# Performance work log

Hardware: AMD Instinct MI355X
Metric: run time of the kernel (lower is better)

Reference implementation:

```python
import jax, jax.numpy as jnp
import numpy as np

T, B, U, A, H, K, G = 800, 128, 64, 64, 256, 10, 20
IN1, IN2, IN3 = 3 + A, 3 + A + H, 3 + A + H


def _lstm_cell(x, h, c, W_ih, W_hh, b):
    # PyTorch LSTMCell: gates in order i, f, g, o
    z = x @ W_ih.T + h @ W_hh.T + b
    i, f, g, o = jnp.split(z, 4, axis=-1)
    c_new = jax.nn.sigmoid(f) * c + jax.nn.sigmoid(i) * jnp.tanh(g)
    h_new = jax.nn.sigmoid(o) * jnp.tanh(c_new)
    return h_new, c_new


def setup_inputs() -> dict:
    key = jax.random.key(0)
    ks = jax.random.split(key, 32)
    s = 0.08
    p = {}
    p['x'] = jax.random.normal(ks[0], (T, B, 3), jnp.float32)
    p['c'] = jax.random.uniform(ks[1], (B, U, A), jnp.float32)
    p['W1_ih'] = jax.random.normal(ks[2], (4 * H, IN1), jnp.float32) * s
    p['W1_hh'] = jax.random.normal(ks[3], (4 * H, H), jnp.float32) * s
    p['b1'] = jax.random.normal(ks[4], (4 * H,), jnp.float32) * s
    p['W2_ih'] = jax.random.normal(ks[5], (4 * H, IN2), jnp.float32) * s
    p['W2_hh'] = jax.random.normal(ks[6], (4 * H, H), jnp.float32) * s
    p['b2'] = jax.random.normal(ks[7], (4 * H,), jnp.float32) * s
    p['W3_ih'] = jax.random.normal(ks[8], (4 * H, IN3), jnp.float32) * s
    p['W3_hh'] = jax.random.normal(ks[9], (4 * H, H), jnp.float32) * s
    p['b3'] = jax.random.normal(ks[10], (4 * H,), jnp.float32) * s
    p['Ww'] = jax.random.normal(ks[11], (3 * K, H), jnp.float32) * s
    p['bw'] = jax.random.normal(ks[12], (3 * K,), jnp.float32) * s
    p['We'] = jax.random.normal(ks[13], (1, H), jnp.float32) * s
    p['be'] = jax.random.normal(ks[14], (1,), jnp.float32) * s
    p['Wpi'] = jax.random.normal(ks[15], (G, H), jnp.float32) * s
    p['bpi'] = jax.random.normal(ks[16], (G,), jnp.float32) * s
    p['Wm1'] = jax.random.normal(ks[17], (G, H), jnp.float32) * s
    p['bm1'] = jax.random.normal(ks[18], (G,), jnp.float32) * s
    p['Wm2'] = jax.random.normal(ks[19], (G, H), jnp.float32) * s
    p['bm2'] = jax.random.normal(ks[20], (G,), jnp.float32) * s
    p['Ws1'] = jax.random.normal(ks[21], (G, H), jnp.float32) * s
    p['bs1'] = jax.random.normal(ks[22], (G,), jnp.float32) * s
    p['Ws2'] = jax.random.normal(ks[23], (G, H), jnp.float32) * s
    p['bs2'] = jax.random.normal(ks[24], (G,), jnp.float32) * s
    p['Wr'] = jax.random.normal(ks[25], (G, H), jnp.float32) * s
    p['br'] = jax.random.normal(ks[26], (G,), jnp.float32) * s
    return p


def reference(x, c, W1_ih, W1_hh, b1, W2_ih, W2_hh, b2, W3_ih, W3_hh, b3,
              Ww, bw, We, be, Wpi, bpi, Wm1, bm1, Wm2, bm2,
              Ws1, bs1, Ws2, bs2, Wr, br):
    u = jnp.arange(U, dtype=x.dtype)  # character positions

    def step(carry, x_t):
        h1, c1, h2, c2, h3, c3, w, kappa = carry
        h1, c1 = _lstm_cell(jnp.concatenate([x_t, w], 1), h1, c1, W1_ih, W1_hh, b1)
        win = jnp.exp(h1 @ Ww.T + bw)                     # [B, 3K]
        alpha, beta, k = jnp.split(win, 3, axis=1)
        kappa = 0.1 * k + kappa                           # [B, K]
        # Phi[b,u] = sum_k alpha * exp(-beta * (kappa - u)^2)
        d = kappa[:, None, :] - u[None, :, None]          # [B, U, K]
        phi = jnp.sum(alpha[:, None, :] * jnp.exp(-beta[:, None, :] * d * d), -1)  # [B, U]
        w = jnp.einsum('bu,bua->ba', phi, c)              # [B, A]
        h2, c2 = _lstm_cell(jnp.concatenate([x_t, w, h1], 1), h2, c2, W2_ih, W2_hh, b2)
        h3, c3 = _lstm_cell(jnp.concatenate([x_t, w, h2], 1), h3, c3, W3_ih, W3_hh, b3)
        return (h1, c1, h2, c2, h3, c3, w, kappa), h3

    z = jnp.zeros((B, H), x.dtype)
    init = (z, z, z, z, z, z, jnp.ones((B, A), x.dtype), jnp.zeros((B, K), x.dtype))
    _, out = jax.lax.scan(step, init, x)                  # out: [T, B, H]

    es = jax.nn.sigmoid(-(out @ We.T + be)).squeeze(-1)   # 1/(1+exp(z)) == sigmoid(-z)
    pis = jax.nn.softmax(out @ Wpi.T + bpi, axis=2)
    mu1s = out @ Wm1.T + bm1
    mu2s = out @ Wm2.T + bm2
    sigma1s = jnp.exp(out @ Ws1.T + bs1)
    sigma2s = jnp.exp(out @ Ws2.T + bs2)
    rhos = jnp.tanh(out @ Wr.T + br)
    return es, pis, mu1s, mu2s, sigma1s, sigma2s, rhos
```

## Files before the change

kernel.cpp:

```cpp
#include <hip/hip_runtime.h>
#include <utility>

#define TT 800
#define BB 128
#define HH 256
#define UU 64
#define AA 64
#define KK 10
#define GG 20
#define NWG 256
#define GB 32
#define NGRP 4

typedef float f32x4 __attribute__((ext_vector_type(4)));
typedef __bf16 bf16y8 __attribute__((ext_vector_type(8)));
typedef short bf16s8 __attribute__((ext_vector_type(8)));
typedef unsigned long long u64x2 __attribute__((ext_vector_type(2)));

__device__ __forceinline__ float bf2f(unsigned short u) {
  return __uint_as_float(((unsigned int)u) << 16);
}
__device__ __forceinline__ unsigned short f2bf(float f) {
  unsigned int x = __float_as_uint(f);
  x += 0x7FFFu + ((x >> 16) & 1u);
  return (unsigned short)(x >> 16);
}
__device__ __forceinline__ unsigned packf(float v) {
  unsigned short hi = f2bf(v);
  unsigned short lo = f2bf(v - bf2f(hi));
  return (unsigned)hi | ((unsigned)lo << 16);
}
__device__ __forceinline__ float unpackf(unsigned u) {
  return bf2f((unsigned short)(u & 0xFFFF)) + bf2f((unsigned short)(u >> 16));
}
__device__ __forceinline__ float sigm(float x) { return 1.0f / (1.0f + __expf(-x)); }
__device__ __forceinline__ float rin(const void* p, size_t i, bool f32) {
  return f32 ? ((const float*)p)[i] : bf2f(((const unsigned short*)p)[i]);
}
__device__ __forceinline__ bf16y8 ld8(const unsigned short* p) {
  return __builtin_bit_cast(bf16y8, *(const bf16s8*)p);
}

__device__ __forceinline__ unsigned ald(const unsigned* p) {
  return __hip_atomic_load(p, __ATOMIC_RELAXED, __HIP_MEMORY_SCOPE_AGENT);
}
__device__ __forceinline__ void ast(unsigned* p, unsigned v) {
  __hip_atomic_store(p, v, __ATOMIC_RELAXED, __HIP_MEMORY_SCOPE_AGENT);
}

__device__ __forceinline__ void ld16(u64x2& d, const unsigned* p) {
  asm volatile("global_load_dwordx4 %0, %1, off sc0 sc1" : "=v"(d) : "v"(p));
}
template <int N>
__device__ __forceinline__ void waitvm() {
  asm volatile("s_waitcnt vmcnt(%0)" :: "i"(N) : "memory");
  __builtin_amdgcn_sched_barrier(0);
}

template <typename F, int... I>
__device__ __forceinline__ void unroll_seq(F&& f, std::integer_sequence<int, I...>) {
  (f(std::integral_constant<int, I>{}), ...);
}


struct KArgs {
  const void* in[27];
  float* out;
  float* kappa;
  unsigned *xu;
  unsigned *wu;
  unsigned *h1[2], *h2[2], *h3[2];
  unsigned* bar;
};

__device__ void fillB(unsigned short* Bhi, unsigned short* Blo, const void* Wih,
                      const void* Whh, int KP, int ihCols, int ihEnd, int hhStart,
                      int q, int tid, bool f32) {
  int total = KP * 16;
  for (int idx = tid; idx < total; idx += 256) {
    int k = idx >> 4, n = idx & 15;
    int row = (n >> 2) * HH + q * 4 + (n & 3);
    float v = 0.f;
    if (k < 3) v = rin(Wih, (size_t)row * ihCols + k, f32);
    else if (k >= 8 && k < ihEnd) v = rin(Wih, (size_t)row * ihCols + (k - 5), f32);
    else if (k >= hhStart && k < hhStart + 256) v = rin(Whh, (size_t)row * HH + (k - hhStart), f32);
    unsigned short hi = f2bf(v);
    int a = ((k >> 3) * 16 + n) * 8 + (k & 7);
    Bhi[a] = hi;
    Blo[a] = f2bf(v - bf2f(hi));
  }
}

template <int KC, bool R3, int WB>
__device__ __forceinline__ void gate_mfma(
    const unsigned* __restrict__ xt, const unsigned* __restrict__ wu,
    const unsigned* __restrict__ r2, const unsigned* __restrict__ r3,
    const unsigned* __restrict__ dz,
    const unsigned short* __restrict__ Bhi, const unsigned short* __restrict__ Blo,
    const float* __restrict__ bias4, float& creg, unsigned* __restrict__ hout,
    int grp, int q, float* zls, int tid) {
  const int wave = tid >> 6, lane = tid & 63;
  if ((wave >> 1) != (WB >> 1)) return;
  const int wv = wave & 1;
  const int n15 = lane & 15, quad = lane >> 4;
  const int b = grp * GB + wv * 16 + n15;

  unsigned xv0 = 0, xv1 = 0, xv2 = 0;
  if (quad == 0) {
    xv0 = xt[b * 3 + 0];
    xv1 = xt[b * 3 + 1];
    xv2 = xt[b * 3 + 2];
  }
  asm volatile("" :: "v"(xv0), "v"(xv1), "v"(xv2));

  constexpr int DEP = 12;
  u64x2 buf[DEP][2];

  auto addr = [&](int kc) -> const unsigned* {
    const int k0 = kc * 32 + quad * 8;
    if (kc == 0 && quad == 0) return dz;
    if (k0 < 72) return wu + ((k0 - 8) >> 3) * 1024 + b * 8;
    if (k0 < 328) return r2 + ((k0 - 72) >> 3) * 1024 + b * 8;
    if (R3 && k0 < 584) return r3 + ((k0 - 328) >> 3) * 1024 + b * 8;
    return dz;
  };
  auto issue = [&](int kc, int slot) {
    const unsigned* p = addr(kc);
    ld16(buf[slot][0], p);
    ld16(buf[slot][1], p + 4);
  };

#pragma unroll
  for (int kc = 0; kc < DEP && kc < KC; ++kc) issue(kc, kc);

  f32x4 acc = {0.f, 0.f, 0.f, 0.f};

  unroll_seq([&](auto kcc) {
    constexpr int kc = decltype(kcc)::value;
    constexpr int end = (kc + DEP < KC) ? (kc + DEP) : KC;
    waitvm<2 * (end - kc - 1)>();
    u64x2* sp = buf[kc % DEP];
    unsigned long long s[4] = { sp[0][0], sp[0][1], sp[1][0], sp[1][1] };
    bf16s8 th, tl;
#pragma unroll
    for (int j = 0; j < 4; ++j) {
      unsigned lo32 = (unsigned)s[j], hi32 = (unsigned)(s[j] >> 32);
      th[2 * j] = (short)(lo32 & 0xFFFFu);     tl[2 * j] = (short)(lo32 >> 16);
      th[2 * j + 1] = (short)(hi32 & 0xFFFFu); tl[2 * j + 1] = (short)(hi32 >> 16);
    }
    if constexpr (kc == 0) {
      if (quad == 0) {
        th[0] = (short)(xv0 & 0xFFFFu); tl[0] = (short)(xv0 >> 16);
        th[1] = (short)(xv1 & 0xFFFFu); tl[1] = (short)(xv1 >> 16);
        th[2] = (short)(xv2 & 0xFFFFu); tl[2] = (short)(xv2 >> 16);
      }
    }
    bf16y8 ah = __builtin_bit_cast(bf16y8, th);
    bf16y8 al = __builtin_bit_cast(bf16y8, tl);
    const int boff = ((kc * 4 + quad) * 16 + n15) * 8;
    bf16y8 bh = ld8(Bhi + boff), bl = ld8(Blo + boff);
    acc = __builtin_amdgcn_mfma_f32_16x16x32_bf16(ah, bh, acc, 0, 0, 0);
    acc = __builtin_amdgcn_mfma_f32_16x16x32_bf16(ah, bl, acc, 0, 0, 0);
    acc = __builtin_amdgcn_mfma_f32_16x16x32_bf16(al, bh, acc, 0, 0, 0);
    if constexpr (kc + DEP < KC) issue(kc + DEP, kc % DEP);
  }, std::make_integer_sequence<int, KC>{});

  float* zw = zls + wave * (16 * 17);
#pragma unroll
  for (int r = 0; r < 4; ++r) zw[(quad * 4 + r) * 17 + n15] = acc[r];
  const int m = lane >> 2, j = lane & 3;
  const int hu = q * 4 + j;
  const int bb = grp * GB + wv * 16 + m;
  float zi = zw[m * 17 + (0 + j)]  + bias4[0];
  float zf = zw[m * 17 + (4 + j)]  + bias4[1];
  float zg = zw[m * 17 + (8 + j)]  + bias4[2];
  float zo = zw[m * 17 + (12 + j)] + bias4[3];
  float cn = sigm(zf) * creg + sigm(zi) * tanhf(zg);
  creg = cn;
  float hn = sigm(zo) * tanhf(cn);
  ast(hout + (hu >> 3) * 1024 + bb * 8 + (hu & 7), packf(hn));
}

template <int kc> constexpr int lw_wait() {
  return kc == 0 ? 4 : kc == 1 ? 2 : kc == 2 ? 0 :
         kc == 15 ? 6 : kc == 16 ? 4 : kc == 17 ? 2 : kc == 18 ? 0 : -1;
}
__device__ __forceinline__ void gate_mfma_lw(
    const unsigned* __restrict__ xt, const unsigned* __restrict__ wu,
    const unsigned* __restrict__ r2, const unsigned* __restrict__ r3,
    const unsigned* __restrict__ dz,
    const unsigned short* __restrict__ Bhi, const unsigned short* __restrict__ Blo,
    const float* __restrict__ bias4, float& creg, unsigned* __restrict__ hout,
    const unsigned* __restrict__ afl, unsigned tgt,
    int grp, int q, float* zls, int tid) {
  constexpr int KC = 19, DEP = 12;
  const int wave = tid >> 6, lane = tid & 63;
  if (wave >= 2) return;
  const int wv = wave & 1;
  const int n15 = lane & 15, quad = lane >> 4;
  const int b = grp * GB + wv * 16 + n15;

  unsigned xv0 = 0, xv1 = 0, xv2 = 0;
  if (quad == 0) {
    xv0 = xt[b * 3 + 0];
    xv1 = xt[b * 3 + 1];
    xv2 = xt[b * 3 + 2];
  }
  asm volatile("" :: "v"(xv0), "v"(xv1), "v"(xv2));

  u64x2 buf[DEP][2];
  u64x2 wbuf[3][2];

  auto addr = [&](int kc) -> const unsigned* {
    const int k0 = kc * 32 + quad * 8;
    if (kc == 0 && quad == 0) return dz;
    if (k0 < 72) return wu + ((k0 - 8) >> 3) * 1024 + b * 8;
    if (k0 < 328) return r2 + ((k0 - 72) >> 3) * 1024 + b * 8;
    if (k0 < 584) return r3 + ((k0 - 328) >> 3) * 1024 + b * 8;
    return dz;
  };
  auto issue = [&](int kc, int slot) {
    const unsigned* p = addr(kc);
    ld16(buf[slot][0], p);
    ld16(buf[slot][1], p + 4);
  };

#pragma unroll
  for (int kc = 3; kc < 15; ++kc) issue(kc, kc % DEP);

  {
    const unsigned* fp = afl + (lane & 31) * 32;
    unsigned v = ald(fp);
    while (v < tgt) { __builtin_amdgcn_s_sleep(1); v = ald(fp); }
  }

#pragma unroll
  for (int kc = 0; kc < 3; ++kc) {
    const unsigned* p = addr(kc);
    ld16(wbuf[kc][0], p);
    ld16(wbuf[kc][1], p + 4);
  }

  f32x4 acc = {0.f, 0.f, 0.f, 0.f};

  unroll_seq([&](auto kcc) {
    constexpr int kc = decltype(kcc)::value;
    constexpr int wn = lw_wait<kc>();
    if constexpr (wn >= 0) waitvm<wn>();
    u64x2* sp = (kc < 3) ? wbuf[kc] : buf[kc % DEP];
    unsigned long long s[4] = { sp[0][0], sp[0][1], sp[1][0], sp[1][1] };
    bf16s8 th, tl;
#pragma unroll
    for (int j = 0; j < 4; ++j) {
      unsigned lo32 = (unsigned)s[j], hi32 = (unsigned)(s[j] >> 32);
      th[2 * j] = (short)(lo32 & 0xFFFFu);     tl[2 * j] = (short)(lo32 >> 16);
      th[2 * j + 1] = (short)(hi32 & 0xFFFFu); tl[2 * j + 1] = (short)(hi32 >> 16);
    }
    if constexpr (kc == 0) {
      if (quad == 0) {
        th[0] = (short)(xv0 & 0xFFFFu); tl[0] = (short)(xv0 >> 16);
        th[1] = (short)(xv1 & 0xFFFFu); tl[1] = (short)(xv1 >> 16);
        th[2] = (short)(xv2 & 0xFFFFu); tl[2] = (short)(xv2 >> 16);
      }
    }
    bf16y8 ah = __builtin_bit_cast(bf16y8, th);
    bf16y8 al = __builtin_bit_cast(bf16y8, tl);
    const int boff = ((kc * 4 + quad) * 16 + n15) * 8;
    bf16y8 bh = ld8(Bhi + boff), bl = ld8(Blo + boff);
    acc = __builtin_amdgcn_mfma_f32_16x16x32_bf16(ah, bh, acc, 0, 0, 0);
    acc = __builtin_amdgcn_mfma_f32_16x16x32_bf16(ah, bl, acc, 0, 0, 0);
    acc = __builtin_amdgcn_mfma_f32_16x16x32_bf16(al, bh, acc, 0, 0, 0);
    if constexpr (kc >= 3 && kc + DEP < KC) issue(kc + DEP, kc % DEP);
  }, std::make_integer_sequence<int, KC>{});

  float* zw = zls + wave * (16 * 17);
#pragma unroll
  for (int r = 0; r < 4; ++r) zw[(quad * 4 + r) * 17 + n15] = acc[r];
  const int m = lane >> 2, j = lane & 3;
  const int hu = q * 4 + j;
  const int bb = grp * GB + wv * 16 + m;
  float zi = zw[m * 17 + (0 + j)]  + bias4[0];
  float zf = zw[m * 17 + (4 + j)]  + bias4[1];
  float zg = zw[m * 17 + (8 + j)]  + bias4[2];
  float zo = zw[m * 17 + (12 + j)] + bias4[3];
  float cn = sigm(zf) * creg + sigm(zi) * tanhf(zg);
  creg = cn;
  float hn = sigm(zo) * tanhf(cn);
  ast(hout + (hu >> 3) * 1024 + bb * 8 + (hu & 7), packf(hn));
}

template <bool F32>
__device__ void window_stage(const KArgs& a, int b, const unsigned* __restrict__ h1c,
                             int tid, float* misc) {
  float* slab = misc;
  float* part = misc + 264;
  float* win  = misc + 508;
  float* kap  = misc + 538;
  float* phi  = misc + 552;
  const int wave = tid >> 6, lane = tid & 63;
  if (wave == 0) {
    const unsigned* p = h1c + (lane >> 1) * 1024 + b * 8 + (lane & 1) * 4;
    u64x2 d;
    ld16(d, p);
    waitvm<0>();
    const int hu0 = (lane >> 1) * 8 + (lane & 1) * 4;
    float* s4 = slab + (hu0 >> 5) * 33 + (hu0 & 31);
    s4[0] = unpackf((unsigned)d[0]);
    s4[1] = unpackf((unsigned)(d[0] >> 32));
    s4[2] = unpackf((unsigned)d[1]);
    s4[3] = unpackf((unsigned)(d[1] >> 32));
  }
  __syncthreads();
  if (tid < 240) {
    int r = tid >> 3, pp = tid & 7;
    const float* hh = slab + pp * 33;
    float s = 0.f;
    if (F32) {
      const f32x4* w4 = (const f32x4*)((const float*)a.in[11] + (size_t)r * HH + pp * 32);
#pragma unroll
      for (int j = 0; j < 8; ++j) {
        f32x4 v = w4[j];
        s += v[0] * hh[4 * j];     s += v[1] * hh[4 * j + 1];
        s += v[2] * hh[4 * j + 2]; s += v[3] * hh[4 * j + 3];
      }
    } else {
      const unsigned short* wr = (const unsigned short*)a.in[11] + (size_t)r * HH + pp * 32;
#pragma unroll
      for (int j = 0; j < 4; ++j) {
        bf16s8 v = *(const bf16s8*)(wr + 8 * j);
#pragma unroll
        for (int e = 0; e < 8; ++e) s += bf2f((unsigned short)v[e]) * hh[8 * j + e];
      }
    }
    part[tid] = s;
  }
  __syncthreads();
  if (tid < 30) {
    float s = rin(a.in[12], tid, F32);
#pragma unroll
    for (int i = 0; i < 8; ++i) s += part[tid * 8 + i];
    win[tid] = __expf(s);
  }
  __syncthreads();
  if (tid < 10) {
    float kp = a.kappa[b * KK + tid] + 0.1f * win[20 + tid];
    a.kappa[b * KK + tid] = kp;
    kap[tid] = kp;
  }
  __syncthreads();
  if (tid < 64) {
    float u = (float)tid, s = 0.f;
#pragma unroll
    for (int r = 0; r < 10; ++r) {
      float d = kap[r] - u;
      s += win[r] * __expf(-win[10 + r] * d * d);
    }
    phi[tid] = s;
  }
  __syncthreads();
  if (tid < 64) {
    float s = 0.f;
    for (int u = 0; u < 64; ++u) s += phi[u] * rin(a.in[1], ((size_t)b * UU + u) * AA + tid, F32);
    ast(a.wu + (tid >> 3) * 1024 + b * 8 + (tid & 7), packf(s));
  }
}

template <bool F32>
__device__ void proj_stage(const KArgs& a, int tt, const unsigned* __restrict__ h3b,
                           int b, int tid, float* misc) {
  float* shm  = misc;
  float* part = misc + 256;
  float* zp   = misc + 500;
  const int wave = tid >> 6, lane = tid & 63;
  if (wave == 0) {
    const unsigned* p = h3b + (lane >> 1) * 1024 + b * 8 + (lane & 1) * 4;
    u64x2 d;
    ld16(d, p);
    waitvm<0>();
    const int hu0 = (lane >> 1) * 8 + (lane & 1) * 4;
    shm[hu0 + 0] = unpackf((unsigned)d[0]);
    shm[hu0 + 1] = unpackf((unsigned)(d[0] >> 32));
    shm[hu0 + 2] = unpackf((unsigned)d[1]);
    shm[hu0 + 3] = unpackf((unsigned)(d[1] >> 32));
  }
  __syncthreads();
  if (tid < 242) {
    int o = tid >> 1, hf = tid & 1;
    const void* Wt;
    const void* bt;
    int rr;
    if (o == 0) {
      Wt = a.in[13]; bt = a.in[14]; rr = 0;
    } else {
      int fam = (o - 1) / 20;
      rr = (o - 1) % 20;
      Wt = a.in[15 + fam * 2];
      bt = a.in[16 + fam * 2];
    }
    float s0 = hf ? 0.f : rin(bt, rr, F32), s1 = 0.f;
    const float* hh = shm + hf * 128;
    if (F32) {
      const f32x4* w4 = (const f32x4*)((const float*)Wt + (size_t)rr * HH + hf * 128);
#pragma unroll 8
      for (int j = 0; j < 32; ++j) {
        f32x4 v = w4[j];
        s0 += v[0] * hh[4 * j];     s1 += v[1] * hh[4 * j + 1];
        s0 += v[2] * hh[4 * j + 2]; s1 += v[3] * hh[4 * j + 3];
      }
    } else {
      const unsigned short* wr = (const unsigned short*)Wt + (size_t)rr * HH + hf * 128;
#pragma unroll 4
      for (int j = 0; j < 16; ++j) {
        bf16s8 v = *(const bf16s8*)(wr + 8 * j);
#pragma unroll
        for (int e = 0; e < 8; e += 2) {
          s0 += bf2f((unsigned short)v[e]) * hh[8 * j + e];
          s1 += bf2f((unsigned short)v[e + 1]) * hh[8 * j + e + 1];
        }
      }
    }
    part[tid] = s0 + s1;
  }
  __syncthreads();
  if (tid < 121) zp[tid] = part[tid * 2] + part[tid * 2 + 1];
  __syncthreads();
  size_t tb = (size_t)tt * BB + b;
  if (tid == 0) {
    a.out[tb] = 1.f / (1.f + __expf(zp[0]));
  } else if (tid < 121) {
    int fam = (tid - 1) / 20, g = (tid - 1) % 20;
    float z = zp[tid];
    float val;
    if (fam == 0) {
      float mx = -1e30f;
      for (int jj = 0; jj < 20; ++jj) mx = fmaxf(mx, zp[1 + jj]);
      float den = 0.f;
      for (int jj = 0; jj < 20; ++jj) den += __expf(zp[1 + jj] - mx);
      val = __expf(z - mx) / den;
    } else if (fam <= 2) {
      val = z;
    } else if (fam <= 4) {
      val = __expf(z);
    } else {
      val = tanhf(z);
    }
    a.out[(size_t)102400 + (size_t)fam * 2048000 + tb * GG + g] = val;
  }
}

#define BAR_WORDS (256 + NWG * 32 + 4096)

__global__ void __launch_bounds__(256) bar_init_kernel(unsigned* bar) {
  for (int i = threadIdx.x; i < BAR_WORDS; i += 256) bar[i] = 0u;
}

__global__ void __launch_bounds__(256, 1) hsm_kernel(KArgs a) {
  __shared__ unsigned short B1h[5632], B1l[5632];
  __shared__ unsigned short B2h[9728], B2l[9728];
  __shared__ unsigned short B3h[9728], B3l[9728];
  __shared__ float zls[4 * 16 * 17];
  __shared__ float misc[768];
  __shared__ unsigned islast;

  const int tid = threadIdx.x;
  const int wg = blockIdx.x;
  const int grp = wg >> 6;
  const int q = wg & 63;
  unsigned* cnt_full = a.bar;
  unsigned* cnt_grp  = a.bar + 32 * (1 + grp);
  unsigned* flags    = a.bar + 256;
  unsigned* myflag   = flags + wg * 32;
  const unsigned* dz = a.bar + 160;
  unsigned* afl = a.bar + 256 + NWG * 32 + grp * 32 * 32;
  unsigned* mya = afl + q * 32;

  auto barrier = [&](unsigned* cnt, unsigned target, unsigned fv, int nfl, int flbase) {
    __syncthreads();
    if (tid == 0) {
      unsigned old = __hip_atomic_fetch_add(cnt, 1u, __ATOMIC_RELAXED,
                                            __HIP_MEMORY_SCOPE_AGENT);
      islast = (old == target - 1u) ? 1u : 0u;
    }
    __syncthreads();
    if (islast) {
      if (tid < nfl) ast(flags + (flbase + tid) * 32, fv);
    } else if (tid == 0) {
      while (ald(myflag) < fv) __builtin_amdgcn_s_sleep(2);
    }
    __syncthreads();
  };

  bool isf32;
  {
    const unsigned short* w = (const unsigned short*)a.in[3];
    int cnt = 0;
    for (int i = 0; i < 128; ++i) {
      float v = bf2f(w[i]);
      if (!(fabsf(v) <= 100.f)) cnt++;
    }
    isf32 = (cnt > 0);
  }

  const int g0 = wg * 256 + tid, gs = 65536;
  if (isf32) {
    const float* xp = (const float*)a.in[0];
    for (int i = g0; i < 307200; i += gs) ast(a.xu + i, packf(xp[i]));
  } else {
    const unsigned short* xp = (const unsigned short*)a.in[0];
    for (int i = g0; i < 307200; i += gs) ast(a.xu + i, (unsigned)xp[i]);
  }
  if (g0 < 32768) {
    ast(a.h1[0] + g0, 0u); ast(a.h1[1] + g0, 0u);
    ast(a.h2[0] + g0, 0u); ast(a.h2[1] + g0, 0u);
    ast(a.h3[0] + g0, 0u); ast(a.h3[1] + g0, 0u);
  }
  if (g0 < 8192) ast(a.wu + g0, 0x00003F80u);
  if (q < GB && tid < KK) a.kappa[(grp * GB + q) * KK + tid] = 0.f;

  float bs1[4], bs2[4], bs3[4];
  {
    const int hu = q * 4 + (tid & 3);
#pragma unroll
    for (int g = 0; g < 4; ++g) {
      bs1[g] = rin(a.in[4], g * HH + hu, isf32);
      bs2[g] = rin(a.in[7], g * HH + hu, isf32);
      bs3[g] = rin(a.in[10], g * HH + hu, isf32);
    }
  }
  float c1r = 0.f, c2r = 0.f, c3r = 0.f;

  fillB(B1h, B1l, a.in[2], a.in[3], 352, 67, 72, 72, q, tid, isf32);
  fillB(B2h, B2l, a.in[5], a.in[6], 608, 323, 328, 328, q, tid, isf32);
  fillB(B3h, B3l, a.in[8], a.in[9], 608, 323, 328, 328, q, tid, isf32);
  barrier(cnt_full, NWG, 1, NWG, 0);

  unsigned ph = 0;

  gate_mfma<11, false, 2>(a.xu, a.wu, a.h1[0], nullptr, dz, B1h, B1l, bs1, c1r,
                          a.h1[1], grp, q, zls, tid);
  ++ph; barrier(cnt_grp, ph * 64u, ph + 1u, 64, grp * 64);

  for (int t = 0; t < TT; ++t) {
    const int p = t & 1;
    const unsigned* xt = a.xu + (size_t)t * BB * 3;
    if (q < GB) {
      if (isf32) window_stage<true>(a, grp * GB + q, a.h1[1 - p], tid, misc);
      else       window_stage<false>(a, grp * GB + q, a.h1[1 - p], tid, misc);
      __syncthreads();
      if (tid == 0) ast(mya, (unsigned)(t + 1));
    } else if (t > 0) {
      if (isf32) proj_stage<true>(a, t - 1, a.h3[p], grp * GB + q - GB, tid, misc);
      else       proj_stage<false>(a, t - 1, a.h3[p], grp * GB + q - GB, tid, misc);
    }
    gate_mfma_lw(xt, a.wu, a.h1[1 - p], a.h2[p], dz, B2h, B2l,
                 bs2, c2r, a.h2[1 - p], afl, (unsigned)(t + 1), grp, q, zls, tid);
    ++ph; barrier(cnt_grp, ph * 64u, ph + 1u, 64, grp * 64);
    gate_mfma<19, true, 0>(xt, a.wu, a.h2[1 - p], a.h3[p], dz, B3h, B3l,
                           bs3, c3r, a.h3[1 - p], grp, q, zls, tid);
    if (t < TT - 1) {
      gate_mfma<11, false, 2>(xt + BB * 3, a.wu, a.h1[1 - p], nullptr, dz,
                              B1h, B1l, bs1, c1r, a.h1[p], grp, q, zls, tid);
    }
    ++ph; barrier(cnt_grp, ph * 64u, ph + 1u, 64, grp * 64);
  }
  if (q >= GB) {
    if (isf32) proj_stage<true>(a, TT - 1, a.h3[0], grp * GB + q - GB, tid, misc);
    else       proj_stage<false>(a, TT - 1, a.h3[0], grp * GB + q - GB, tid, misc);
  }
}

extern "C" void kernel_launch(void* const* d_in, const int* in_sizes, int n_in,
                              void* d_out, int out_size, void* d_ws, size_t ws_size,
                              hipStream_t stream) {
  KArgs a;
  for (int i = 0; i < 27; ++i) a.in[i] = d_in[i];
  a.out = (float*)d_out;

  char* ws = (char*)d_ws;
  size_t off = 0;
  auto take = [&](size_t bytes) {
    void* p = ws + off;
    off = (off + bytes + 127) & ~(size_t)127;
    return p;
  };
  a.kappa = (float*)take(1280 * 4);
  a.wu    = (unsigned*)take(8192 * 4);
  a.h1[0] = (unsigned*)take(32768 * 4);
  a.h1[1] = (unsigned*)take(32768 * 4);
  a.h2[0] = (unsigned*)take(32768 * 4);
  a.h2[1] = (unsigned*)take(32768 * 4);
  a.h3[0] = (unsigned*)take(32768 * 4);
  a.h3[1] = (unsigned*)take(32768 * 4);
  a.xu    = (unsigned*)take(307200 * 4);
  a.bar   = (unsigned*)take(BAR_WORDS * 4);

  bar_init_kernel<<<1, 256, 0, stream>>>(a.bar);
  hsm_kernel<<<NWG, 256, 0, stream>>>(a);
}
```

Baseline: 12.50 ms.

## Replace mid-step group barrier with per-workgroup flags and overlap layer-1 gates

Each timestep previously ran two group-wide barriers. Now layer-2 completion is published through per-workgroup flags (cfl), and layer 3 polls those flags before loading the h2 inputs, so one of the two barriers is removed. The next step's layer-1 gate computation moves onto waves 2-3 and polls the window flags, so it runs concurrently with layer 2 on waves 0-1. This shortens the serial critical path per timestep, at the cost of extra flag memory, spin-polling, and subtle memory-ordering assumptions (a vmcnt drain before the relaxed flag stores).

```diff
diff --git a/kernel.cpp b/kernel.cpp
--- a/kernel.cpp
+++ b/kernel.cpp
@@ -56,6 +56,18 @@
   asm volatile("s_waitcnt vmcnt(%0)" :: "i"(N) : "memory");
   __builtin_amdgcn_sched_barrier(0);
 }
+__device__ __forceinline__ void vdrain() {
+  __builtin_amdgcn_sched_barrier(0);
+  asm volatile("s_waitcnt vmcnt(0)" ::: "memory");
+  __builtin_amdgcn_sched_barrier(0);
+}
+
+__device__ __forceinline__ void pollN(const unsigned* fl, int mask, unsigned tgt,
+                                      int lane) {
+  const unsigned* fp = fl + (lane & mask) * 32;
+  unsigned v = ald(fp);
+  while (v < tgt) { __builtin_amdgcn_s_sleep(1); v = ald(fp); }
+}
 
 template <typename F, int... I>
 __device__ __forceinline__ void unroll_seq(F&& f, std::integer_sequence<int, I...>) {
@@ -72,6 +84,17 @@
   unsigned *h1[2], *h2[2], *h3[2];
   unsigned* bar;
 };
+
+__device__ __forceinline__ const unsigned* addrA(int kc, int quad, int b,
+    const unsigned* wu, const unsigned* r2, const unsigned* r3, bool R3v,
+    const unsigned* dz) {
+  const int k0 = kc * 32 + quad * 8;
+  if (kc == 0 && quad == 0) return dz;
+  if (k0 < 72) return wu + ((k0 - 8) >> 3) * 1024 + b * 8;
+  if (k0 < 328) return r2 + ((k0 - 72) >> 3) * 1024 + b * 8;
+  if (R3v && k0 < 584) return r3 + ((k0 - 328) >> 3) * 1024 + b * 8;
+  return dz;
+}
 
 __device__ void fillB(unsigned short* Bhi, unsigned short* Blo, const void* Wih,
                       const void* Whh, int KP, int ihCols, int ihEnd, int hhStart,
@@ -91,6 +114,52 @@
   }
 }
 
+__device__ __forceinline__ void kc_mfma(f32x4& acc, const unsigned long long* s,
+    bool inj, unsigned xv0, unsigned xv1, unsigned xv2, int kc, int quad, int n15,
+    const unsigned short* Bhi, const unsigned short* Blo) {
+  bf16s8 th, tl;
+#pragma unroll
+  for (int j = 0; j < 4; ++j) {
+    unsigned lo32 = (unsigned)s[j], hi32 = (unsigned)(s[j] >> 32);
+    th[2 * j] = (short)(lo32 & 0xFFFFu);     tl[2 * j] = (short)(lo32 >> 16);
+    th[2 * j + 1] = (short)(hi32 & 0xFFFFu); tl[2 * j + 1] = (short)(hi32 >> 16);
+  }
+  if (inj) {
+    th[0] = (short)(xv0 & 0xFFFFu); tl[0] = (short)(xv0 >> 16);
+    th[1] = (short)(xv1 & 0xFFFFu); tl[1] = (short)(xv1 >> 16);
+    th[2] = (short)(xv2 & 0xFFFFu); tl[2] = (short)(xv2 >> 16);
+  }
+  bf16y8 ah = __builtin_bit_cast(bf16y8, th);
+  bf16y8 al = __builtin_bit_cast(bf16y8, tl);
+  const int boff = ((kc * 4 + quad) * 16 + n15) * 8;
+  bf16y8 bh = ld8(Bhi + boff), bl = ld8(Blo + boff);
+  acc = __builtin_amdgcn_mfma_f32_16x16x32_bf16(ah, bh, acc, 0, 0, 0);
+  acc = __builtin_amdgcn_mfma_f32_16x16x32_bf16(ah, bl, acc, 0, 0, 0);
+  acc = __builtin_amdgcn_mfma_f32_16x16x32_bf16(al, bh, acc, 0, 0, 0);
+}
+
+__device__ __forceinline__ void gate_epi(f32x4 acc, const float* bias4,
+    float& creg, unsigned* hout, int grp, int q, float* zls, int wave, int lane) {
+  const int wv = wave & 1, n15 = lane & 15, quad = lane >> 4;
+  float* zw = zls + wave * (16 * 17);
+#pragma unroll
+  for (int r = 0; r < 4; ++r) zw[(quad * 4 + r) * 17 + n15] = acc[r];
+  __builtin_amdgcn_sched_barrier(0);
+  asm volatile("s_waitcnt lgkmcnt(0)" ::: "memory");
+  __builtin_amdgcn_sched_barrier(0);
+  const int m = lane >> 2, j = lane & 3;
+  const int hu = q * 4 + j;
+  const int bb = grp * GB + wv * 16 + m;
+  float zi = zw[m * 17 + (0 + j)]  + bias4[0];
+  float zf = zw[m * 17 + (4 + j)]  + bias4[1];
+  float zg = zw[m * 17 + (8 + j)]  + bias4[2];
+  float zo = zw[m * 17 + (12 + j)] + bias4[3];
+  float cn = sigm(zf) * creg + sigm(zi) * tanhf(zg);
+  creg = cn;
+  float hn = sigm(zo) * tanhf(cn);
+  ast(hout + (hu >> 3) * 1024 + bb * 8 + (hu & 7), packf(hn));
+}
+
 template <int KC, bool R3, int WB>
 __device__ __forceinline__ void gate_mfma(
     const unsigned* __restrict__ xt, const unsigned* __restrict__ wu,
@@ -107,78 +176,31 @@
 
   unsigned xv0 = 0, xv1 = 0, xv2 = 0;
   if (quad == 0) {
-    xv0 = xt[b * 3 + 0];
-    xv1 = xt[b * 3 + 1];
-    xv2 = xt[b * 3 + 2];
+    xv0 = xt[b * 3 + 0]; xv1 = xt[b * 3 + 1]; xv2 = xt[b * 3 + 2];
   }
   asm volatile("" :: "v"(xv0), "v"(xv1), "v"(xv2));
 
   constexpr int DEP = 12;
   u64x2 buf[DEP][2];
-
-  auto addr = [&](int kc) -> const unsigned* {
-    const int k0 = kc * 32 + quad * 8;
-    if (kc == 0 && quad == 0) return dz;
-    if (k0 < 72) return wu + ((k0 - 8) >> 3) * 1024 + b * 8;
-    if (k0 < 328) return r2 + ((k0 - 72) >> 3) * 1024 + b * 8;
-    if (R3 && k0 < 584) return r3 + ((k0 - 328) >> 3) * 1024 + b * 8;
-    return dz;
+  auto issue = [&](int kc, int slot) {
+    const unsigned* p = addrA(kc, quad, b, wu, r2, r3, R3, dz);
+    ld16(buf[slot][0], p); ld16(buf[slot][1], p + 4);
   };
-  auto issue = [&](int kc, int slot) {
-    const unsigned* p = addr(kc);
-    ld16(buf[slot][0], p);
-    ld16(buf[slot][1], p + 4);
-  };
-
 #pragma unroll
   for (int kc = 0; kc < DEP && kc < KC; ++kc) issue(kc, kc);
 
   f32x4 acc = {0.f, 0.f, 0.f, 0.f};
-
   unroll_seq([&](auto kcc) {
     constexpr int kc = decltype(kcc)::value;
     constexpr int end = (kc + DEP < KC) ? (kc + DEP) : KC;
     waitvm<2 * (end - kc - 1)>();
     u64x2* sp = buf[kc % DEP];
     unsigned long long s[4] = { sp[0][0], sp[0][1], sp[1][0], sp[1][1] };
-    bf16s8 th, tl;
-#pragma unroll
-    for (int j = 0; j < 4; ++j) {
-      unsigned lo32 = (unsigned)s[j], hi32 = (unsigned)(s[j] >> 32);
-      th[2 * j] = (short)(lo32 & 0xFFFFu);     tl[2 * j] = (short)(lo32 >> 16);
-      th[2 * j + 1] = (short)(hi32 & 0xFFFFu); tl[2 * j + 1] = (short)(hi32 >> 16);
-    }
-    if constexpr (kc == 0) {
-      if (quad == 0) {
-        th[0] = (short)(xv0 & 0xFFFFu); tl[0] = (short)(xv0 >> 16);
-        th[1] = (short)(xv1 & 0xFFFFu); tl[1] = (short)(xv1 >> 16);
-        th[2] = (short)(xv2 & 0xFFFFu); tl[2] = (short)(xv2 >> 16);
-      }
-    }
-    bf16y8 ah = __builtin_bit_cast(bf16y8, th);
-    bf16y8 al = __builtin_bit_cast(bf16y8, tl);
-    const int boff = ((kc * 4 + quad) * 16 + n15) * 8;
-    bf16y8 bh = ld8(Bhi + boff), bl = ld8(Blo + boff);
-    acc = __builtin_amdgcn_mfma_f32_16x16x32_bf16(ah, bh, acc, 0, 0, 0);
-    acc = __builtin_amdgcn_mfma_f32_16x16x32_bf16(ah, bl, acc, 0, 0, 0);
-    acc = __builtin_amdgcn_mfma_f32_16x16x32_bf16(al, bh, acc, 0, 0, 0);
+    kc_mfma(acc, s, kc == 0 && quad == 0, xv0, xv1, xv2, kc, quad, n15, Bhi, Blo);
     if constexpr (kc + DEP < KC) issue(kc + DEP, kc % DEP);
   }, std::make_integer_sequence<int, KC>{});
 
-  float* zw = zls + wave * (16 * 17);
-#pragma unroll
-  for (int r = 0; r < 4; ++r) zw[(quad * 4 + r) * 17 + n15] = acc[r];
-  const int m = lane >> 2, j = lane & 3;
-  const int hu = q * 4 + j;
-  const int bb = grp * GB + wv * 16 + m;
-  float zi = zw[m * 17 + (0 + j)]  + bias4[0];
-  float zf = zw[m * 17 + (4 + j)]  + bias4[1];
-  float zg = zw[m * 17 + (8 + j)]  + bias4[2];
-  float zo = zw[m * 17 + (12 + j)] + bias4[3];
-  float cn = sigm(zf) * creg + sigm(zi) * tanhf(zg);
-  creg = cn;
-  float hn = sigm(zo) * tanhf(cn);
-  ast(hout + (hu >> 3) * 1024 + bb * 8 + (hu & 7), packf(hn));
+  gate_epi(acc, bias4, creg, hout, grp, q, zls, wave, lane);
 }
 
 template <int kc> constexpr int lw_wait() {
@@ -202,91 +224,142 @@
 
   unsigned xv0 = 0, xv1 = 0, xv2 = 0;
   if (quad == 0) {
-    xv0 = xt[b * 3 + 0];
-    xv1 = xt[b * 3 + 1];
-    xv2 = xt[b * 3 + 2];
+    xv0 = xt[b * 3 + 0]; xv1 = xt[b * 3 + 1]; xv2 = xt[b * 3 + 2];
   }
   asm volatile("" :: "v"(xv0), "v"(xv1), "v"(xv2));
 
   u64x2 buf[DEP][2];
   u64x2 wbuf[3][2];
-
-  auto addr = [&](int kc) -> const unsigned* {
-    const int k0 = kc * 32 + quad * 8;
-    if (kc == 0 && quad == 0) return dz;
-    if (k0 < 72) return wu + ((k0 - 8) >> 3) * 1024 + b * 8;
-    if (k0 < 328) return r2 + ((k0 - 72) >> 3) * 1024 + b * 8;
-    if (k0 < 584) return r3 + ((k0 - 328) >> 3) * 1024 + b * 8;
-    return dz;
+  auto issue = [&](int kc, int slot) {
+    const unsigned* p = addrA(kc, quad, b, wu, r2, r3, true, dz);
+    ld16(buf[slot][0], p); ld16(buf[slot][1], p + 4);
   };
-  auto issue = [&](int kc, int slot) {
-    const unsigned* p = addr(kc);
-    ld16(buf[slot][0], p);
-    ld16(buf[slot][1], p + 4);
-  };
 
 #pragma unroll
   for (int kc = 3; kc < 15; ++kc) issue(kc, kc % DEP);
 
-  {
-    const unsigned* fp = afl + (lane & 31) * 32;
-    unsigned v = ald(fp);
-    while (v < tgt) { __builtin_amdgcn_s_sleep(1); v = ald(fp); }
-  }
+  pollN(afl, 31, tgt, lane);
 
 #pragma unroll
   for (int kc = 0; kc < 3; ++kc) {
-    const unsigned* p = addr(kc);
-    ld16(wbuf[kc][0], p);
-    ld16(wbuf[kc][1], p + 4);
+    const unsigned* p = addrA(kc, quad, b, wu, r2, r3, true, dz);
+    ld16(wbuf[kc][0], p); ld16(wbuf[kc][1], p + 4);
   }
 
   f32x4 acc = {0.f, 0.f, 0.f, 0.f};
-
   unroll_seq([&](auto kcc) {
     constexpr int kc = decltype(kcc)::value;
     constexpr int wn = lw_wait<kc>();
     if constexpr (wn >= 0) waitvm<wn>();
     u64x2* sp = (kc < 3) ? wbuf[kc] : buf[kc % DEP];
     unsigned long long s[4] = { sp[0][0], sp[0][1], sp[1][0], sp[1][1] };
-    bf16s8 th, tl;
-#pragma unroll
-    for (int j = 0; j < 4; ++j) {
-      unsigned lo32 = (unsigned)s[j], hi32 = (unsigned)(s[j] >> 32);
-      th[2 * j] = (short)(lo32 & 0xFFFFu);     tl[2 * j] = (short)(lo32 >> 16);
-      th[2 * j + 1] = (short)(hi32 & 0xFFFFu); tl[2 * j + 1] = (short)(hi32 >> 16);
-    }
-    if constexpr (kc == 0) {
-      if (quad == 0) {
-        th[0] = (short)(xv0 & 0xFFFFu); tl[0] = (short)(xv0 >> 16);
-        th[1] = (short)(xv1 & 0xFFFFu); tl[1] = (short)(xv1 >> 16);
-        th[2] = (short)(xv2 & 0xFFFFu); tl[2] = (short)(xv2 >> 16);
-      }
-    }
-    bf16y8 ah = __builtin_bit_cast(bf16y8, th);
-    bf16y8 al = __builtin_bit_cast(bf16y8, tl);
-    const int boff = ((kc * 4 + quad) * 16 + n15) * 8;
-    bf16y8 bh = ld8(Bhi + boff), bl = ld8(Blo + boff);
-    acc = __builtin_amdgcn_mfma_f32_16x16x32_bf16(ah, bh, acc, 0, 0, 0);
-    acc = __builtin_amdgcn_mfma_f32_16x16x32_bf16(ah, bl, acc, 0, 0, 0);
-    acc = __builtin_amdgcn_mfma_f32_16x16x32_bf16(al, bh, acc, 0, 0, 0);
+    kc_mfma(acc, s, kc == 0 && quad == 0, xv0, xv1, xv2, kc, quad, n15, Bhi, Blo);
     if constexpr (kc >= 3 && kc + DEP < KC) issue(kc + DEP, kc % DEP);
   }, std::make_integer_sequence<int, KC>{});
 
-  float* zw = zls + wave * (16 * 17);
-#pragma unroll
-  for (int r = 0; r < 4; ++r) zw[(quad * 4 + r) * 17 + n15] = acc[r];
-  const int m = lane >> 2, j = lane & 3;
-  const int hu = q * 4 + j;
-  const int bb = grp * GB + wv * 16 + m;
-  float zi = zw[m * 17 + (0 + j)]  + bias4[0];
-  float zf = zw[m * 17 + (4 + j)]  + bias4[1];
-  float zg = zw[m * 17 + (8 + j)]  + bias4[2];
-  float zo = zw[m * 17 + (12 + j)] + bias4[3];
-  float cn = sigm(zf) * creg + sigm(zi) * tanhf(zg);
-  creg = cn;
-  float hn = sigm(zo) * tanhf(cn);
-  ast(hout + (hu >> 3) * 1024 + bb * 8 + (hu & 7), packf(hn));
+  gate_epi(acc, bias4, creg, hout, grp, q, zls, wave, lane);
+}
+
+__device__ __forceinline__ void gate_mfma_lw11(
+    const unsigned* __restrict__ xt, const unsigned* __restrict__ wu,
+    const unsigned* __restrict__ r2, const unsigned* __restrict__ dz,
+    const unsigned short* __restrict__ Bhi, const unsigned short* __restrict__ Blo,
+    const float* __restrict__ bias4, float& creg, unsigned* __restrict__ hout,
+    const unsigned* __restrict__ afl, unsigned tgt,
+    int grp, int q, float* zls, int tid) {
+  constexpr int KC = 11;
+  const int wave = tid >> 6, lane = tid & 63;
+  if (wave < 2) return;
+  const int n15 = lane & 15, quad = lane >> 4;
+  const int b = grp * GB + (wave & 1) * 16 + n15;
+
+  unsigned xv0 = 0, xv1 = 0, xv2 = 0;
+  if (quad == 0) {
+    xv0 = xt[b * 3 + 0]; xv1 = xt[b * 3 + 1]; xv2 = xt[b * 3 + 2];
+  }
+  asm volatile("" :: "v"(xv0), "v"(xv1), "v"(xv2));
+
+  u64x2 buf[8][2];
+  u64x2 wbuf[3][2];
+#pragma unroll
+  for (int kc = 3; kc < KC; ++kc) {
+    const unsigned* p = addrA(kc, quad, b, wu, r2, dz, false, dz);
+    ld16(buf[kc - 3][0], p); ld16(buf[kc - 3][1], p + 4);
+  }
+
+  pollN(afl, 31, tgt, lane);
+
+#pragma unroll
+  for (int kc = 0; kc < 3; ++kc) {
+    const unsigned* p = addrA(kc, quad, b, wu, r2, dz, false, dz);
+    ld16(wbuf[kc][0], p); ld16(wbuf[kc][1], p + 4);
+  }
+
+  f32x4 acc = {0.f, 0.f, 0.f, 0.f};
+  unroll_seq([&](auto kcc) {
+    constexpr int kc = decltype(kcc)::value;
+    if constexpr (kc == 0) waitvm<4>();
+    else if constexpr (kc == 1) waitvm<2>();
+    else if constexpr (kc == 2) waitvm<0>();
+    u64x2* sp = (kc < 3) ? wbuf[kc] : buf[kc - 3];
+    unsigned long long s[4] = { sp[0][0], sp[0][1], sp[1][0], sp[1][1] };
+    kc_mfma(acc, s, kc == 0 && quad == 0, xv0, xv1, xv2, kc, quad, n15, Bhi, Blo);
+  }, std::make_integer_sequence<int, KC>{});
+
+  gate_epi(acc, bias4, creg, hout, grp, q, zls, wave, lane);
+}
+
+__device__ __forceinline__ void gate_mfma_lh2(
+    const unsigned* __restrict__ xt, const unsigned* __restrict__ wu,
+    const unsigned* __restrict__ r2, const unsigned* __restrict__ r3,
+    const unsigned* __restrict__ dz,
+    const unsigned short* __restrict__ Bhi, const unsigned short* __restrict__ Blo,
+    const float* __restrict__ bias4, float& creg, unsigned* __restrict__ hout,
+    const unsigned* __restrict__ cfl, unsigned tgt,
+    int grp, int q, float* zls, int tid) {
+  constexpr int KC = 19;
+  const int wave = tid >> 6, lane = tid & 63;
+  if (wave >= 2) return;
+  const int wv = wave & 1;
+  const int n15 = lane & 15, quad = lane >> 4;
+  const int b = grp * GB + wv * 16 + n15;
+
+  unsigned xv0 = 0, xv1 = 0, xv2 = 0;
+  if (quad == 0) {
+    xv0 = xt[b * 3 + 0]; xv1 = xt[b * 3 + 1]; xv2 = xt[b * 3 + 2];
+  }
+  asm volatile("" :: "v"(xv0), "v"(xv1), "v"(xv2));
+
+  u64x2 buf[KC][2];
+#pragma unroll
+  for (int kc = 0; kc < 2; ++kc) {
+    const unsigned* p = addrA(kc, quad, b, wu, r2, r3, true, dz);
+    ld16(buf[kc][0], p); ld16(buf[kc][1], p + 4);
+  }
+#pragma unroll
+  for (int kc = 11; kc < 19; ++kc) {
+    const unsigned* p = addrA(kc, quad, b, wu, r2, r3, true, dz);
+    ld16(buf[kc][0], p); ld16(buf[kc][1], p + 4);
+  }
+
+  pollN(cfl, 63, tgt, lane);
+
+#pragma unroll
+  for (int kc = 2; kc <= 10; ++kc) {
+    const unsigned* p = addrA(kc, quad, b, wu, r2, r3, true, dz);
+    ld16(buf[kc][0], p); ld16(buf[kc][1], p + 4);
+  }
+
+  f32x4 acc = {0.f, 0.f, 0.f, 0.f};
+  unroll_seq([&](auto kcc) {
+    constexpr int kc = decltype(kcc)::value;
+    if constexpr (kc >= 2 && kc <= 10) waitvm<2 * (10 - kc)>();
+    u64x2* sp = buf[kc];
+    unsigned long long s[4] = { sp[0][0], sp[0][1], sp[1][0], sp[1][1] };
+    kc_mfma(acc, s, kc == 0 && quad == 0, xv0, xv1, xv2, kc, quad, n15, Bhi, Blo);
+  }, std::make_integer_sequence<int, KC>{});
+
+  gate_epi(acc, bias4, creg, hout, grp, q, zls, wave, lane);
 }
 
 template <bool F32>
@@ -448,7 +521,7 @@
   }
 }
 
-#define BAR_WORDS (256 + NWG * 32 + 4096)
+#define BAR_WORDS (256 + NWG * 32 + 4096 + NGRP * 64 * 32)
 
 __global__ void __launch_bounds__(256) bar_init_kernel(unsigned* bar) {
   for (int i = threadIdx.x; i < BAR_WORDS; i += 256) bar[i] = 0u;
@@ -461,11 +534,13 @@
   __shared__ float zls[4 * 16 * 17];
   __shared__ float misc[768];
   __shared__ unsigned islast;
+  __shared__ unsigned c2w1;
 
   const int tid = threadIdx.x;
   const int wg = blockIdx.x;
   const int grp = wg >> 6;
   const int q = wg & 63;
+  const int wave = tid >> 6, lane = tid & 63;
   unsigned* cnt_full = a.bar;
   unsigned* cnt_grp  = a.bar + 32 * (1 + grp);
   unsigned* flags    = a.bar + 256;
@@ -473,6 +548,8 @@
   const unsigned* dz = a.bar + 160;
   unsigned* afl = a.bar + 256 + NWG * 32 + grp * 32 * 32;
   unsigned* mya = afl + q * 32;
+  unsigned* cfl = a.bar + 256 + NWG * 32 + 4096 + grp * 64 * 32;
+  unsigned* myc = cfl + q * 32;
 
   auto barrier = [&](unsigned* cnt, unsigned target, unsigned fv, int nfl, int flbase) {
     __syncthreads();
@@ -501,6 +578,7 @@
     isf32 = (cnt > 0);
   }
 
+  if (tid == 0) c2w1 = 0u;
   const int g0 = wg * 256 + tid, gs = 65536;
   if (isf32) {
     const float* xp = (const float*)a.in[0];
@@ -543,26 +621,48 @@
   for (int t = 0; t < TT; ++t) {
     const int p = t & 1;
     const unsigned* xt = a.xu + (size_t)t * BB * 3;
+    const unsigned* h1c = a.h1[1 - p];
+    const unsigned tv = (unsigned)(t + 1);
+
     if (q < GB) {
-      if (isf32) window_stage<true>(a, grp * GB + q, a.h1[1 - p], tid, misc);
-      else       window_stage<false>(a, grp * GB + q, a.h1[1 - p], tid, misc);
-      __syncthreads();
-      if (tid == 0) ast(mya, (unsigned)(t + 1));
+      if (isf32) window_stage<true>(a, grp * GB + q, h1c, tid, misc);
+      else       window_stage<false>(a, grp * GB + q, h1c, tid, misc);
+      if (wave == 0) {
+        vdrain();
+        if (lane == 0) ast(mya, tv);
+      }
     } else if (t > 0) {
       if (isf32) proj_stage<true>(a, t - 1, a.h3[p], grp * GB + q - GB, tid, misc);
       else       proj_stage<false>(a, t - 1, a.h3[p], grp * GB + q - GB, tid, misc);
     }
-    gate_mfma_lw(xt, a.wu, a.h1[1 - p], a.h2[p], dz, B2h, B2l,
-                 bs2, c2r, a.h2[1 - p], afl, (unsigned)(t + 1), grp, q, zls, tid);
+
+    if (wave < 2) {
+      gate_mfma_lw(xt, a.wu, h1c, a.h2[p], dz, B2h, B2l,
+                   bs2, c2r, a.h2[1 - p], afl, tv, grp, q, zls, tid);
+      vdrain();
+      if (wave == 1) {
+        if (lane == 0)
+          __hip_atomic_store(&c2w1, tv, __ATOMIC_RELAXED, __HIP_MEMORY_SCOPE_WORKGROUP);
+      } else {
+        if (lane == 0) {
+          while (__hip_atomic_load(&c2w1, __ATOMIC_RELAXED,
+                                   __HIP_MEMORY_SCOPE_WORKGROUP) < tv)
+            __builtin_amdgcn_s_sleep(1);
+          ast(myc, tv);
+        }
+      }
+    } else if (t < TT - 1) {
+      gate_mfma_lw11(xt + BB * 3, a.wu, h1c, dz, B1h, B1l, bs1, c1r,
+                     a.h1[p], afl, tv, grp, q, zls, tid);
+    }
+
+    if (wave < 2) {
+      gate_mfma_lh2(xt, a.wu, a.h2[1 - p], a.h3[p], dz, B3h, B3l,
+                    bs3, c3r, a.h3[1 - p], cfl, tv, grp, q, zls, tid);
+    }
     ++ph; barrier(cnt_grp, ph * 64u, ph + 1u, 64, grp * 64);
-    gate_mfma<19, true, 0>(xt, a.wu, a.h2[1 - p], a.h3[p], dz, B3h, B3l,
-                           bs3, c3r, a.h3[1 - p], grp, q, zls, tid);
-    if (t < TT - 1) {
-      gate_mfma<11, false, 2>(xt + BB * 3, a.wu, a.h1[1 - p], nullptr, dz,
-                              B1h, B1l, bs1, c1r, a.h1[p], grp, q, zls, tid);
-    }
-    ++ph; barrier(cnt_grp, ph * 64u, ph + 1u, 64, grp * 64);
-  }
+  }
+
   if (q >= GB) {
     if (isf32) proj_stage<true>(a, TT - 1, a.h3[0], grp * GB + q - GB, tid, misc);
     else       proj_stage<false>(a, TT - 1, a.h3[0], grp * GB + q - GB, tid, misc);
```

Result: slower. 14.20 ms (+13.6%).
